# Kernel optimization log

Hardware: AMD Instinct MI355X
Metric: run time of the kernel (lower is better)

The kernel has to match this reference:

```python
import jax, jax.numpy as jnp
import numpy as np

B = 8192       # batch
HID = 1024     # hidden_dim
HEADS = 8      # head_count
OBS, ACT, N_AGENTS = 128, 32, 4
ENC_IN = N_AGENTS * OBS + ACT   # 544
DEC_IN = (N_AGENTS - 1) * ACT   # 96


def _linear(key, fan_in, fan_out):
    k1, k2 = jax.random.split(key)
    lim = 1.0 / np.sqrt(fan_in)
    W = jax.random.uniform(k1, (fan_in, fan_out), minval=-lim, maxval=lim, dtype=jnp.float32)
    b = jax.random.uniform(k2, (fan_out,), minval=-lim, maxval=lim, dtype=jnp.float32)
    return W, b


def setup_inputs() -> dict:
    key = jax.random.key(0)
    ks = jax.random.split(key, 10)
    s = jax.random.normal(ks[0], (B, N_AGENTS * OBS), dtype=jnp.float32)
    a = jax.random.normal(ks[1], (B, N_AGENTS * ACT), dtype=jnp.float32)
    W_enc_in, b_enc_in = _linear(ks[2], ENC_IN, HID)   # encoder_input_fc
    W_dec_in, b_dec_in = _linear(ks[3], DEC_IN, HID)   # decoder_input_fc
    W_eh, b_eh = _linear(ks[4], HID, HID)              # fc_encoder_input
    head_ks = jax.random.split(ks[5], HEADS)
    Wb = [_linear(k, HID, HID) for k in head_ks]       # fc_encoder_heads
    W_heads = jnp.stack([w for w, _ in Wb], axis=0)    # [H, HID, HID]
    b_heads = jnp.stack([b for _, b in Wb], axis=0)    # [H, HID]
    W_dh, b_dh = _linear(ks[6], HID, HID)              # fc_decoder_input
    W1, b1 = _linear(ks[7], HID, HID)                  # fc1
    W2, b2 = _linear(ks[8], HID, 1)                    # fc2
    return {"s": s, "a": a,
            "W_enc_in": W_enc_in, "b_enc_in": b_enc_in,
            "W_dec_in": W_dec_in, "b_dec_in": b_dec_in,
            "W_eh": W_eh, "b_eh": b_eh,
            "W_heads": W_heads, "b_heads": b_heads,
            "W_dh": W_dh, "b_dh": b_dh,
            "W1": W1, "b1": b1, "W2": W2, "b2": b2}


def reference(s, a, W_enc_in, b_enc_in, W_dec_in, b_dec_in, W_eh, b_eh,
              W_heads, b_heads, W_dh, b_dh, W1, b1, W2, b2):
    relu = jax.nn.relu
    # agent id = 0: own action is a[:, :ACT], others' actions are a[:, ACT:]
    enc_input = jnp.concatenate([s, a[:, :ACT]], axis=1) @ W_enc_in + b_enc_in   # [B, HID]
    dec_input = a[:, ACT:] @ W_dec_in + b_dec_in                                 # [B, HID]
    # Attention_ATT_2
    encoder_h = relu(enc_input @ W_eh + b_eh)                                    # [B, HID]
    encoder_heads = relu(jnp.einsum('bd,hde->hbe', encoder_h, W_heads)
                         + b_heads[:, None, :])                                  # [H, B, HID]
    decoder_H = relu(dec_input @ W_dh + b_dh)                                    # [B, HID]
    scores = jnp.einsum('hbd,bd->bh', encoder_heads, decoder_H)                  # [B, H]
    attn = jax.nn.softmax(scores, axis=1)                                        # [B, H]
    context = jnp.einsum('hbd,bh->bd', encoder_heads, attn)                      # [B, HID]
    x = relu(context @ W1 + b1)
    q = x @ W2 + b2                                                              # [B, 1]
    return q
```

## Files before the change

kernel.cpp:

```cpp
#include <hip/hip_runtime.h>
#include <hip/hip_bf16.h>
#include <hip/hip_fp16.h>

#define BATCH   8192
#define HID     1024
#define HEADS   8
#define BC      2048

typedef unsigned int  u32;
typedef unsigned short u16;
typedef __attribute__((ext_vector_type(8))) short bf16x8;
typedef __attribute__((ext_vector_type(4))) float f32x4;

__device__ __forceinline__ u32 pack_hi2(u32 u0, u32 u1) {
    return (u0 >> 16) | (u1 & 0xFFFF0000u);
}
__device__ __forceinline__ void split1(float x, u16& h, u16& l) {
    const u32 u = __float_as_uint(x);
    h = (u16)(u >> 16);
    const float r = x - __uint_as_float(u & 0xFFFF0000u);
    l = (u16)(__float_as_uint(r) >> 16);
}
__device__ __forceinline__ void splitA4(float4 v, uint2& hi, uint2& lo) {
    u32 u0 = __float_as_uint(v.x), u1 = __float_as_uint(v.y),
        u2 = __float_as_uint(v.z), u3 = __float_as_uint(v.w);
    float r0 = v.x - __uint_as_float(u0 & 0xFFFF0000u);
    float r1 = v.y - __uint_as_float(u1 & 0xFFFF0000u);
    float r2 = v.z - __uint_as_float(u2 & 0xFFFF0000u);
    float r3 = v.w - __uint_as_float(u3 & 0xFFFF0000u);
    hi.x = pack_hi2(u0, u1);
    hi.y = pack_hi2(u2, u3);
    lo.x = pack_hi2(__float_as_uint(r0), __float_as_uint(r1));
    lo.y = pack_hi2(__float_as_uint(r2), __float_as_uint(r3));
}

__device__ __forceinline__ void gld16(const u16* g, u16* l) {
    __builtin_amdgcn_global_load_lds(
        (const __attribute__((address_space(1))) u32*)g,
        (__attribute__((address_space(3))) u32*)l, 16, 0, 0);
}

struct WSplitArgs {
    const float* src[6];
    u16* hi[6];
    u16* lo[6];
};

__global__ __launch_bounds__(256) void split_weight_all(WSplitArgs args)
{
    const int z = blockIdx.z;
    int which, zz = 0;
    if (z < 3)       { which = z; }
    else if (z < 11) { which = 3; zz = z - 3; }
    else             { which = z - 7; }
    const int KT = (which == 4) ? 17 : (which == 5 ? 3 : 32);
    const int kt = blockIdx.x;
    if (kt >= KT) return;
    const int K = KT * 32;
    const long long zoff = (long long)zz * K * 1024;
    const float* W  = args.src[which] + zoff;
    u16* hi = args.hi[which] + zoff;
    u16* lo = args.lo[which] + zoff;

    const int n0  = blockIdx.y * 128;
    const int tid = threadIdx.x;
    const int k   = tid >> 3;
    const int ng  = (tid & 7) * 16;
    const float* src = W + (long long)(kt * 32 + k) * 1024 + n0 + ng;
    u16* dh = hi + ((long long)kt * 1024 + n0) * 32 + k;
    u16* dl = lo + ((long long)kt * 1024 + n0) * 32 + k;
#pragma unroll
    for (int t = 0; t < 4; t++) {
        const float4 v = *(const float4*)(src + t * 4);
        u16 h0, l0, h1, l1, h2, l2, h3, l3;
        split1(v.x, h0, l0); split1(v.y, h1, l1);
        split1(v.z, h2, l2); split1(v.w, h3, l3);
        const int nb = (ng + t * 4) * 32;
        dh[nb]      = h0; dl[nb]      = l0;
        dh[nb + 32] = h1; dl[nb + 32] = l1;
        dh[nb + 64] = h2; dl[nb + 64] = l2;
        dh[nb + 96] = h3; dl[nb + 96] = l3;
    }
}

#define HYB_GEOM \
    const int tid  = threadIdx.x; \
    const int lane = tid & 63; \
    const int wv   = tid >> 6; \
    const int wm   = wv >> 1, wn = wv & 1; \
    const int fr   = lane & 15; \
    const int fq   = lane >> 4; \
    const int m0   = blockIdx.y * 128; \
    const int n0   = blockIdx.x * 128; \
    const int lro2 = (lane >> 2) * 32 + (((lane & 3) ^ ((lane >> 3) & 3)) * 8); \
    const int br0  = wv * 16; \
    const int br1  = 64 + wv * 16; \
    const int fqx2 = (fq ^ ((fr >> 1) & 3)) * 8;

#define STAGE_HI(Ahp_, Bhp_, aoff_, boff_) \
    { \
        const u16* Ag_ = (Ahp_) + (aoff_); \
        const u16* Bg_ = (Bhp_) + (boff_); \
        gld16(Ag_ + br0 * 32 + lro2, &Ah[br0 * 32]); \
        gld16(Ag_ + br1 * 32 + lro2, &Ah[br1 * 32]); \
        gld16(Bg_ + br0 * 32 + lro2, &Bh[br0 * 32]); \
        gld16(Bg_ + br1 * 32 + lro2, &Bh[br1 * 32]); \
    }

#define LOAD_LO(Alp_, Blp_, aoff_, boff_, al_, bl_) \
    { \
        const u16* Al_ = (Alp_) + (aoff_); \
        const u16* Bl_ = (Blp_) + (boff_); \
        _Pragma("unroll") \
        for (int i = 0; i < 4; i++) { \
            al_[i] = *(const bf16x8*)(Al_ + (wm * 64 + i * 16 + fr) * 32 + fq * 8); \
            bl_[i] = *(const bf16x8*)(Bl_ + (wn * 64 + i * 16 + fr) * 32 + fq * 8); \
        } \
    }

#define MFMA_SLAB16(acc_, al_, bl_) \
    { \
        bf16x8 ah[4], bh[4]; \
        _Pragma("unroll") \
        for (int i = 0; i < 4; i++) { \
            ah[i] = *(const bf16x8*)&Ah[(wm * 64 + i * 16 + fr) * 32 + fqx2]; \
            bh[i] = *(const bf16x8*)&Bh[(wn * 64 + i * 16 + fr) * 32 + fqx2]; \
        } \
        _Pragma("unroll") \
        for (int i = 0; i < 4; i++) \
            _Pragma("unroll") \
            for (int j = 0; j < 4; j++) { \
                acc_[i][j] = __builtin_amdgcn_mfma_f32_16x16x32_bf16(ah[i], bh[j], acc_[i][j], 0, 0, 0); \
                acc_[i][j] = __builtin_amdgcn_mfma_f32_16x16x32_bf16(ah[i], bl_[j], acc_[i][j], 0, 0, 0); \
                acc_[i][j] = __builtin_amdgcn_mfma_f32_16x16x32_bf16(al_[i], bh[j], acc_[i][j], 0, 0, 0); \
            } \
    }

template <int RELU, int OUTP>
__global__ __launch_bounds__(256) void gemm_fast(
    const u16* __restrict__ Ahp, const u16* __restrict__ Alp, int MA, int moff,
    const u16* __restrict__ Bhp, const u16* __restrict__ Blp,
    const float* __restrict__ bias,
    float* __restrict__ Cf,
    u16* __restrict__ Chp, u16* __restrict__ Clp, int MC,
    int K)
{
    __shared__ alignas(16) u16 Ah[4096], Bh[4096];
    HYB_GEOM

    f32x4 acc[4][4];
#pragma unroll
    for (int i = 0; i < 4; i++)
#pragma unroll
        for (int j = 0; j < 4; j++) acc[i][j] = 0;

    const int KT = K >> 5;
    for (int kt = 0; kt < KT; kt++) {
        const long long aoff = ((long long)kt * MA + moff + m0) * 32;
        const long long boff = ((long long)kt * 1024 + n0) * 32;
        STAGE_HI(Ahp, Bhp, aoff, boff);
        bf16x8 al[4], bl[4];
        LOAD_LO(Alp, Blp, aoff, boff, al, bl);
        __syncthreads();
        MFMA_SLAB16(acc, al, bl);
        __syncthreads();
    }

#pragma unroll
    for (int j = 0; j < 4; j++) {
        const int n = n0 + wn * 64 + j * 16 + fr;
        const float bb = bias[n];
#pragma unroll
        for (int i = 0; i < 4; i++) {
#pragma unroll
            for (int r = 0; r < 4; r++) {
                const int m = m0 + wm * 64 + i * 16 + fq * 4 + r;
                float v = acc[i][j][r] + bb;
                if (RELU) v = fmaxf(v, 0.0f);
                if (OUTP) {
                    u16 h, l;
                    split1(v, h, l);
                    const long long d = ((long long)(n >> 5) * MC + moff + m) * 32 + (n & 31);
                    Chp[d] = h;
                    Clp[d] = l;
                } else {
                    Cf[(long long)m * 1024 + n] = v;
                }
            }
        }
    }
}

template <int RELU>
__global__ __launch_bounds__(256) void gemm_cvt(
    const float* __restrict__ src1, int lda1, int kofs1,
    const float* __restrict__ src2, int lda2, int ksplit,
    const u16* __restrict__ Bhp, const u16* __restrict__ Blp,
    const float* __restrict__ bias,
    u16* __restrict__ Chp, u16* __restrict__ Clp, int MC,
    int K)
{
    __shared__ alignas(16) u16 Ah[4096], Al[4096], Bh[4096], Bl[4096];
    const int tid  = threadIdx.x;
    const int lane = tid & 63;
    const int wv   = tid >> 6;
    const int wm   = wv >> 1, wn = wv & 1;
    const int fr   = lane & 15;
    const int fq   = lane >> 4;
    const int m0   = blockIdx.y * 128;
    const int n0   = blockIdx.x * 128;
    const int fqx  = (fq ^ (fr & 3)) * 8;
    const int lro  = (lane >> 2) * 32 + (((lane & 3) ^ ((lane >> 2) & 3)) * 8);
    const int br0  = wv * 16;
    const int br1  = 64 + wv * 16;
    const int ar   = tid >> 3;
    const int akq  = tid & 7;
    const int awoff = (((akq >> 1) ^ (ar & 3)) * 8) + (akq & 1) * 4;

    f32x4 acc[4][4];
#pragma unroll
    for (int i = 0; i < 4; i++)
#pragma unroll
        for (int j = 0; j < 4; j++) acc[i][j] = 0;

    const int KT = K >> 5;
    for (int kt = 0; kt < KT; kt++) {
        const int k0 = kt * 32;
        const float* srcp; int ldk, kc;
        if (k0 < ksplit) { srcp = src1; ldk = lda1; kc = k0 + kofs1; }
        else             { srcp = src2; ldk = lda2; kc = k0 - ksplit; }

        const u16* Bg  = Bhp + ((long long)kt * 1024 + n0) * 32;
        const u16* Bg2 = Blp + ((long long)kt * 1024 + n0) * 32;
        gld16(Bg  + br0 * 32 + lro, &Bh[br0 * 32]);
        gld16(Bg  + br1 * 32 + lro, &Bh[br1 * 32]);
        gld16(Bg2 + br0 * 32 + lro, &Bl[br0 * 32]);
        gld16(Bg2 + br1 * 32 + lro, &Bl[br1 * 32]);

#pragma unroll
        for (int it = 0; it < 4; it++) {
            const int row = ar + it * 32;
            const float4 v = *(const float4*)(srcp + (long long)(m0 + row) * ldk + kc + akq * 4);
            uint2 hi, lo;
            splitA4(v, hi, lo);
            *(uint2*)&Ah[row * 32 + awoff] = hi;
            *(uint2*)&Al[row * 32 + awoff] = lo;
        }
        __syncthreads();

        bf16x8 ah[4], al[4], bh[4], bl[4];
#pragma unroll
        for (int i = 0; i < 4; i++) {
            const int off = (wm * 64 + i * 16 + fr) * 32 + fqx;
            ah[i] = *(const bf16x8*)&Ah[off];
            al[i] = *(const bf16x8*)&Al[off];
        }
#pragma unroll
        for (int j = 0; j < 4; j++) {
            const int off = (wn * 64 + j * 16 + fr) * 32 + fqx;
            bh[j] = *(const bf16x8*)&Bh[off];
            bl[j] = *(const bf16x8*)&Bl[off];
        }
#pragma unroll
        for (int i = 0; i < 4; i++)
#pragma unroll
            for (int j = 0; j < 4; j++) {
                acc[i][j] = __builtin_amdgcn_mfma_f32_16x16x32_bf16(ah[i], bh[j], acc[i][j], 0, 0, 0);
                acc[i][j] = __builtin_amdgcn_mfma_f32_16x16x32_bf16(ah[i], bl[j], acc[i][j], 0, 0, 0);
                acc[i][j] = __builtin_amdgcn_mfma_f32_16x16x32_bf16(al[i], bh[j], acc[i][j], 0, 0, 0);
            }
        __syncthreads();
    }

#pragma unroll
    for (int j = 0; j < 4; j++) {
        const int n = n0 + wn * 64 + j * 16 + fr;
        const float bb = bias[n];
#pragma unroll
        for (int i = 0; i < 4; i++) {
#pragma unroll
            for (int r = 0; r < 4; r++) {
                const int m = m0 + wm * 64 + i * 16 + fq * 4 + r;
                float v = acc[i][j][r] + bb;
                if (RELU) v = fmaxf(v, 0.0f);
                u16 h, l;
                split1(v, h, l);
                const long long d = ((long long)(n >> 5) * MC + m) * 32 + (n & 31);
                Chp[d] = h;
                Clp[d] = l;
            }
        }
    }
}

__global__ __launch_bounds__(256) void heads_kernel(
    const u16* __restrict__ Ahp, const u16* __restrict__ Alp, int MA, int moff,
    const u16* __restrict__ Whp, const u16* __restrict__ Wlp,
    const float* __restrict__ b_heads,
    const float* __restrict__ decH,
    __half* __restrict__ headsb,
    float* __restrict__ scoresp)
{
    __shared__ alignas(16) u16 Ah[4096], Bh[4096];
    __shared__ float scred[2][128];
    HYB_GEOM
    const int h = blockIdx.z;
    const u16* Bhp = Whp + (long long)h * 1048576;
    const u16* Blp = Wlp + (long long)h * 1048576;
    const float* bias = b_heads + h * 1024;

    f32x4 acc[4][4];
#pragma unroll
    for (int i = 0; i < 4; i++)
#pragma unroll
        for (int j = 0; j < 4; j++) acc[i][j] = 0;

    for (int kt = 0; kt < 32; kt++) {
        const long long aoff = ((long long)kt * MA + moff + m0) * 32;
        const long long boff = ((long long)kt * 1024 + n0) * 32;
        STAGE_HI(Ahp, Bhp, aoff, boff);
        bf16x8 al[4], bl[4];
        LOAD_LO(Alp, Blp, aoff, boff, al, bl);
        __syncthreads();
        MFMA_SLAB16(acc, al, bl);
        __syncthreads();
    }

    float part[4][4];
#pragma unroll
    for (int i = 0; i < 4; i++)
#pragma unroll
        for (int r = 0; r < 4; r++) part[i][r] = 0.0f;

#pragma unroll
    for (int j = 0; j < 4; j++) {
        const int n = n0 + wn * 64 + j * 16 + fr;
        const float bb = bias[n];
#pragma unroll
        for (int i = 0; i < 4; i++) {
#pragma unroll
            for (int r = 0; r < 4; r++) {
                const int b_loc = m0 + wm * 64 + i * 16 + fq * 4 + r;
                const float v = fmaxf(acc[i][j][r] + bb, 0.0f);
                headsb[((long long)b_loc * HEADS + h) * 1024 + n] = __float2half(v);
                part[i][r] = fmaf(v, decH[(long long)b_loc * 1024 + n], part[i][r]);
            }
        }
    }
#pragma unroll
    for (int off = 1; off < 16; off <<= 1)
#pragma unroll
        for (int i = 0; i < 4; i++)
#pragma unroll
            for (int r = 0; r < 4; r++)
                part[i][r] += __shfl_xor(part[i][r], off, 64);

    if (fr == 0) {
#pragma unroll
        for (int i = 0; i < 4; i++)
#pragma unroll
            for (int r = 0; r < 4; r++)
                scred[wn][wm * 64 + i * 16 + fq * 4 + r] = part[i][r];
    }
    __syncthreads();
    if (tid < 128) {
        const float sv = scred[0][tid] + scred[1][tid];
        scoresp[(long long)(h * 8 + blockIdx.x) * BC + m0 + tid] = sv;
    }
}

__global__ __launch_bounds__(256) void context_kernel(
    const __half* __restrict__ headsb, const float* __restrict__ scoresp,
    u16* __restrict__ ctx_hi, u16* __restrict__ ctx_lo, int MC, int row0)
{
    __shared__ float sc_s[64];
    __shared__ float attn_s[HEADS];
    const int b = blockIdx.x;
    const int tid = threadIdx.x;
    if (tid < 64) sc_s[tid] = scoresp[(long long)tid * BC + b];
    __syncthreads();
    if (tid == 0) {
        float sc[HEADS];
#pragma unroll
        for (int h = 0; h < HEADS; h++) {
            float s = 0.0f;
#pragma unroll
            for (int nt = 0; nt < 8; nt++) s += sc_s[h * 8 + nt];
            sc[h] = s;
        }
        float mx = sc[0];
#pragma unroll
        for (int h = 1; h < HEADS; h++) mx = fmaxf(mx, sc[h]);
        float e[HEADS], sum = 0.0f;
#pragma unroll
        for (int h = 0; h < HEADS; h++) { e[h] = __expf(sc[h] - mx); sum += e[h]; }
        const float inv = 1.0f / sum;
#pragma unroll
        for (int h = 0; h < HEADS; h++) attn_s[h] = e[h] * inv;
    }
    __syncthreads();

    const int d = tid * 4;
    float w[HEADS];
#pragma unroll
    for (int h = 0; h < HEADS; h++) w[h] = attn_s[h];
    float4 acc = make_float4(0.f, 0.f, 0.f, 0.f);
#pragma unroll
    for (int h = 0; h < HEADS; h++) {
        const __half2* hp = (const __half2*)(headsb + ((long long)b * HEADS + h) * 1024 + d);
        const float2 f0 = __half22float2(hp[0]);
        const float2 f1 = __half22float2(hp[1]);
        acc.x = fmaf(w[h], f0.x, acc.x);
        acc.y = fmaf(w[h], f0.y, acc.y);
        acc.z = fmaf(w[h], f1.x, acc.z);
        acc.w = fmaf(w[h], f1.y, acc.w);
    }
    uint2 hi, lo;
    splitA4(acc, hi, lo);
    const long long off = ((long long)(d >> 5) * MC + row0 + b) * 32 + (d & 31);
    *(uint2*)(ctx_hi + off) = hi;
    *(uint2*)(ctx_lo + off) = lo;
}

__global__ __launch_bounds__(256) void fc2_kernel(
    const float* __restrict__ x, const float* __restrict__ W2,
    const float* __restrict__ b2, float* __restrict__ q)
{
    const int b   = blockIdx.x;
    const int tid = threadIdx.x;
    __shared__ float red[4];

    const float4 xv = *(const float4*)(x + (long long)b * 1024 + tid * 4);
    const float4 wv = *(const float4*)(W2 + tid * 4);
    float p = xv.x * wv.x + xv.y * wv.y + xv.z * wv.z + xv.w * wv.w;
#pragma unroll
    for (int off = 32; off > 0; off >>= 1) p += __shfl_down(p, off, 64);
    if ((tid & 63) == 0) red[tid >> 6] = p;
    __syncthreads();
    if (tid == 0) q[b] = red[0] + red[1] + red[2] + red[3] + b2[0];
}

extern "C" void kernel_launch(void* const* d_in, const int* in_sizes, int n_in,
                              void* d_out, int out_size, void* d_ws, size_t ws_size,
                              hipStream_t stream)
{
    const float* s        = (const float*)d_in[0];
    const float* a        = (const float*)d_in[1];
    const float* W_enc_in = (const float*)d_in[2];
    const float* b_enc_in = (const float*)d_in[3];
    const float* W_dec_in = (const float*)d_in[4];
    const float* b_dec_in = (const float*)d_in[5];
    const float* W_eh     = (const float*)d_in[6];
    const float* b_eh     = (const float*)d_in[7];
    const float* W_heads  = (const float*)d_in[8];
    const float* b_heads  = (const float*)d_in[9];
    const float* W_dh     = (const float*)d_in[10];
    const float* b_dh     = (const float*)d_in[11];
    const float* W1       = (const float*)d_in[12];
    const float* b1       = (const float*)d_in[13];
    const float* W2       = (const float*)d_in[14];
    const float* b2       = (const float*)d_in[15];
    float* q_out = (float*)d_out;

    u16* P = (u16*)d_ws;
    u16* enc_hi = P; P += 557056;
    u16* enc_lo = P; P += 557056;
    u16* dec_hi = P; P += 98304;
    u16* dec_lo = P; P += 98304;
    u16* eh_hi  = P; P += 1048576;
    u16* eh_lo  = P; P += 1048576;
    u16* dh_hi  = P; P += 1048576;
    u16* dh_lo  = P; P += 1048576;
    u16* w1_hi  = P; P += 1048576;
    u16* w1_lo  = P; P += 1048576;
    u16* wh_hi  = P; P += 8388608;
    u16* wh_lo  = P; P += 8388608;
    char* act = (char*)P;

    const dim3 blk(256);

    WSplitArgs wa;
    wa.src[0] = W_eh;    wa.hi[0] = eh_hi;  wa.lo[0] = eh_lo;
    wa.src[1] = W_dh;    wa.hi[1] = dh_hi;  wa.lo[1] = dh_lo;
    wa.src[2] = W1;      wa.hi[2] = w1_hi;  wa.lo[2] = w1_lo;
    wa.src[3] = W_heads; wa.hi[3] = wh_hi;  wa.lo[3] = wh_lo;
    wa.src[4] = W_enc_in; wa.hi[4] = enc_hi; wa.lo[4] = enc_lo;
    wa.src[5] = W_dec_in; wa.hi[5] = dec_hi; wa.lo[5] = dec_lo;
    split_weight_all<<<dim3(32, 8, 13), blk, 0, stream>>>(wa);

    const bool high = (ws_size >= 150011904ULL);

    if (high) {
        u16*    bufA_hi = (u16*)act;
        u16*    bufA_lo = bufA_hi + 8388608;
        __half* headsb  = (__half*)act;
        u16*    encH_hi = (u16*)(act + 33554432);
        u16*    encH_lo = encH_hi + 8388608;
        float*  decH    = (float*)(act + 2LL * 33554432);
        float*  scoresp = (float*)(act + 3LL * 33554432);

        const dim3 gg(8, 64, 1);
        gemm_cvt<0><<<gg, blk, 0, stream>>>(s, 512, 0, a, 128, 512,
            enc_hi, enc_lo, b_enc_in, bufA_hi, bufA_lo, 8192, 544);
        gemm_fast<1, 1><<<gg, blk, 0, stream>>>(bufA_hi, bufA_lo, 8192, 0,
            eh_hi, eh_lo, b_eh, nullptr, encH_hi, encH_lo, 8192, 1024);
        gemm_cvt<0><<<gg, blk, 0, stream>>>(a, 128, 32, a, 128, 1 << 28,
            dec_hi, dec_lo, b_dec_in, bufA_hi, bufA_lo, 8192, 96);
        gemm_fast<1, 0><<<gg, blk, 0, stream>>>(bufA_hi, bufA_lo, 8192, 0,
            dh_hi, dh_lo, b_dh, decH, nullptr, nullptr, 0, 1024);

        for (int c = 0; c < BATCH / BC; c++) {
            heads_kernel<<<dim3(8, BC / 128, 8), blk, 0, stream>>>(
                encH_hi, encH_lo, 8192, c * BC, wh_hi, wh_lo, b_heads,
                decH + (long long)c * BC * 1024, headsb, scoresp);
            context_kernel<<<dim3(BC), blk, 0, stream>>>(
                headsb, scoresp, encH_hi, encH_lo, 8192, c * BC);
        }
        gemm_fast<1, 0><<<gg, blk, 0, stream>>>(encH_hi, encH_lo, 8192, 0,
            w1_hi, w1_lo, b1, decH, nullptr, nullptr, 0, 1024);
        fc2_kernel<<<dim3(BATCH), blk, 0, stream>>>(decH, W2, b2, q_out);
    } else {
        __half* headsb  = (__half*)act;
        u16*    bufA_hi = (u16*)act;
        u16*    bufA_lo = bufA_hi + 2097152;
        u16*    encH_hi = (u16*)(act + 33554432);
        u16*    encH_lo = encH_hi + 2097152;
        float*  decH    = (float*)(act + 33554432 + 8388608);
        float*  scoresp = (float*)(act + 33554432 + 2LL * 8388608);

        const dim3 gg(8, BC / 128, 1);
        for (int c = 0; c < BATCH / BC; c++) {
            const float* sC = s + (long long)c * BC * 512;
            const float* aC = a + (long long)c * BC * 128;
            gemm_cvt<0><<<gg, blk, 0, stream>>>(sC, 512, 0, aC, 128, 512,
                enc_hi, enc_lo, b_enc_in, bufA_hi, bufA_lo, BC, 544);
            gemm_fast<1, 1><<<gg, blk, 0, stream>>>(bufA_hi, bufA_lo, BC, 0,
                eh_hi, eh_lo, b_eh, nullptr, encH_hi, encH_lo, BC, 1024);
            gemm_cvt<0><<<gg, blk, 0, stream>>>(aC, 128, 32, aC, 128, 1 << 28,
                dec_hi, dec_lo, b_dec_in, bufA_hi, bufA_lo, BC, 96);
            gemm_fast<1, 0><<<gg, blk, 0, stream>>>(bufA_hi, bufA_lo, BC, 0,
                dh_hi, dh_lo, b_dh, decH, nullptr, nullptr, 0, 1024);
            heads_kernel<<<dim3(8, BC / 128, 8), blk, 0, stream>>>(
                encH_hi, encH_lo, BC, 0, wh_hi, wh_lo, b_heads,
                decH, headsb, scoresp);
            context_kernel<<<dim3(BC), blk, 0, stream>>>(
                headsb, scoresp, encH_hi, encH_lo, BC, 0);
            gemm_fast<1, 0><<<gg, blk, 0, stream>>>(encH_hi, encH_lo, BC, 0,
                w1_hi, w1_lo, b1, decH, nullptr, nullptr, 0, 1024);
            fc2_kernel<<<dim3(BC), blk, 0, stream>>>(decH, W2, b2, q_out + (long long)c * BC);
        }
    }
}
```

Before: 779.2 us.

## Triple-buffer LDS pipeline with 256x128 tiles and 512-thread blocks for GEMMs

Replaces the single-buffered synchronous K loop in gemm_fast and heads_kernel with a three-stage LDS ring. Both hi and lo bf16 halves are loaded asynchronously two tiles ahead, and the MFMA phases are split into two half-tiles with barriers and s_setprio. Blocks grow to 512 threads covering 256 rows, which halves the grid and doubles B-tile reuse. This aims to hide global load latency and cut per-iteration sync stalls, at the cost of about 144KB of LDS per block, which limits occupancy to one block per CU and relies on precise vmcnt accounting.

```diff
diff --git a/kernel.cpp b/kernel.cpp
--- a/kernel.cpp
+++ b/kernel.cpp
@@ -83,61 +83,104 @@
     }
 }
 
-#define HYB_GEOM \
+#define PIPE_GEOM \
     const int tid  = threadIdx.x; \
     const int lane = tid & 63; \
     const int wv   = tid >> 6; \
     const int wm   = wv >> 1, wn = wv & 1; \
     const int fr   = lane & 15; \
     const int fq   = lane >> 4; \
-    const int m0   = blockIdx.y * 128; \
+    const int m0   = blockIdx.y * 256; \
     const int n0   = blockIdx.x * 128; \
     const int lro2 = (lane >> 2) * 32 + (((lane & 3) ^ ((lane >> 3) & 3)) * 8); \
-    const int br0  = wv * 16; \
-    const int br1  = 64 + wv * 16; \
-    const int fqx2 = (fq ^ ((fr >> 1) & 3)) * 8;
-
-#define STAGE_HI(Ahp_, Bhp_, aoff_, boff_) \
-    { \
-        const u16* Ag_ = (Ahp_) + (aoff_); \
-        const u16* Bg_ = (Bhp_) + (boff_); \
-        gld16(Ag_ + br0 * 32 + lro2, &Ah[br0 * 32]); \
-        gld16(Ag_ + br1 * 32 + lro2, &Ah[br1 * 32]); \
-        gld16(Bg_ + br0 * 32 + lro2, &Bh[br0 * 32]); \
-        gld16(Bg_ + br1 * 32 + lro2, &Bh[br1 * 32]); \
-    }
-
-#define LOAD_LO(Alp_, Blp_, aoff_, boff_, al_, bl_) \
-    { \
-        const u16* Al_ = (Alp_) + (aoff_); \
-        const u16* Bl_ = (Blp_) + (boff_); \
+    const int fqx2 = (fq ^ ((fr >> 1) & 3)) * 8; \
+    const int wr   = wv * 16;
+
+#define PSTAGE_HI(dst_, aoff_, boff_) { \
+    u16* db_ = (dst_); \
+    gld16(Ahp + (aoff_) + (long long)wr * 32 + lro2, db_ + wr * 32); \
+    gld16(Ahp + (aoff_) + (long long)(128 + wr) * 32 + lro2, db_ + (128 + wr) * 32); \
+    gld16(Bhp + (boff_) + (long long)wr * 32 + lro2, db_ + 16384 + wr * 32); }
+
+#define PSTAGE_LO(dst_, aoff_, boff_) { \
+    u16* db_ = (dst_); \
+    gld16(Alp + (aoff_) + (long long)wr * 32 + lro2, db_ + 8192 + wr * 32); \
+    gld16(Alp + (aoff_) + (long long)(128 + wr) * 32 + lro2, db_ + 8192 + (128 + wr) * 32); \
+    gld16(Blp + (boff_) + (long long)wr * 32 + lro2, db_ + 20480 + wr * 32); }
+
+#define PTILE(t_, STAGE0_, STAGE1_, TAILWAIT_) { \
+    const u16* bufp = smem + ((t_) % 3) * 24576; \
+    bf16x8 bh[4], bl[4], ah0[2], al0[2], ah1[2], al1[2]; \
+    _Pragma("unroll") \
+    for (int j = 0; j < 4; j++) { \
+        const int off = (wn * 64 + j * 16 + fr) * 32 + fqx2; \
+        bh[j] = *(const bf16x8*)(bufp + 16384 + off); \
+        bl[j] = *(const bf16x8*)(bufp + 20480 + off); } \
+    _Pragma("unroll") \
+    for (int i = 0; i < 2; i++) { \
+        const int off = (wm * 64 + i * 16 + fr) * 32 + fqx2; \
+        ah0[i] = *(const bf16x8*)(bufp + off); \
+        al0[i] = *(const bf16x8*)(bufp + 8192 + off); } \
+    STAGE0_; \
+    __builtin_amdgcn_s_barrier(); \
+    __builtin_amdgcn_s_setprio(1); \
+    _Pragma("unroll") \
+    for (int i = 0; i < 2; i++) \
         _Pragma("unroll") \
-        for (int i = 0; i < 4; i++) { \
-            al_[i] = *(const bf16x8*)(Al_ + (wm * 64 + i * 16 + fr) * 32 + fq * 8); \
-            bl_[i] = *(const bf16x8*)(Bl_ + (wn * 64 + i * 16 + fr) * 32 + fq * 8); \
-        } \
-    }
-
-#define MFMA_SLAB16(acc_, al_, bl_) \
-    { \
-        bf16x8 ah[4], bh[4]; \
+        for (int j = 0; j < 4; j++) { \
+            acc[i][j] = __builtin_amdgcn_mfma_f32_16x16x32_bf16(ah0[i], bh[j], acc[i][j], 0, 0, 0); \
+            acc[i][j] = __builtin_amdgcn_mfma_f32_16x16x32_bf16(ah0[i], bl[j], acc[i][j], 0, 0, 0); \
+            acc[i][j] = __builtin_amdgcn_mfma_f32_16x16x32_bf16(al0[i], bh[j], acc[i][j], 0, 0, 0); } \
+    __builtin_amdgcn_s_setprio(0); \
+    __builtin_amdgcn_s_barrier(); \
+    __builtin_amdgcn_sched_barrier(0); \
+    _Pragma("unroll") \
+    for (int i = 0; i < 2; i++) { \
+        const int off = (wm * 64 + (2 + i) * 16 + fr) * 32 + fqx2; \
+        ah1[i] = *(const bf16x8*)(bufp + off); \
+        al1[i] = *(const bf16x8*)(bufp + 8192 + off); } \
+    STAGE1_; \
+    __builtin_amdgcn_s_barrier(); \
+    __builtin_amdgcn_s_setprio(1); \
+    _Pragma("unroll") \
+    for (int i = 0; i < 2; i++) \
         _Pragma("unroll") \
-        for (int i = 0; i < 4; i++) { \
-            ah[i] = *(const bf16x8*)&Ah[(wm * 64 + i * 16 + fr) * 32 + fqx2]; \
-            bh[i] = *(const bf16x8*)&Bh[(wn * 64 + i * 16 + fr) * 32 + fqx2]; \
-        } \
-        _Pragma("unroll") \
-        for (int i = 0; i < 4; i++) \
-            _Pragma("unroll") \
-            for (int j = 0; j < 4; j++) { \
-                acc_[i][j] = __builtin_amdgcn_mfma_f32_16x16x32_bf16(ah[i], bh[j], acc_[i][j], 0, 0, 0); \
-                acc_[i][j] = __builtin_amdgcn_mfma_f32_16x16x32_bf16(ah[i], bl_[j], acc_[i][j], 0, 0, 0); \
-                acc_[i][j] = __builtin_amdgcn_mfma_f32_16x16x32_bf16(al_[i], bh[j], acc_[i][j], 0, 0, 0); \
-            } \
-    }
+        for (int j = 0; j < 4; j++) { \
+            acc[2 + i][j] = __builtin_amdgcn_mfma_f32_16x16x32_bf16(ah1[i], bh[j], acc[2 + i][j], 0, 0, 0); \
+            acc[2 + i][j] = __builtin_amdgcn_mfma_f32_16x16x32_bf16(ah1[i], bl[j], acc[2 + i][j], 0, 0, 0); \
+            acc[2 + i][j] = __builtin_amdgcn_mfma_f32_16x16x32_bf16(al1[i], bh[j], acc[2 + i][j], 0, 0, 0); } \
+    __builtin_amdgcn_s_setprio(0); \
+    TAILWAIT_; \
+    __builtin_amdgcn_s_barrier(); \
+    __builtin_amdgcn_sched_barrier(0); \
+}
+
+#define PIPE_LOOP \
+    const int KT = K >> 5; \
+    const long long astep = (long long)MA * 32; \
+    const long long bstep = 32768; \
+    const long long abase = ((long long)moff + m0) * 32; \
+    const long long bbase = (long long)n0 * 32; \
+    PSTAGE_HI(smem, abase, bbase); \
+    PSTAGE_LO(smem, abase, bbase); \
+    PSTAGE_HI(smem + 24576, abase + astep, bbase + bstep); \
+    PSTAGE_LO(smem + 24576, abase + astep, bbase + bstep); \
+    asm volatile("s_waitcnt vmcnt(6)" ::: "memory"); \
+    __builtin_amdgcn_s_barrier(); \
+    __builtin_amdgcn_sched_barrier(0); \
+    for (int t = 0; t < KT - 2; t++) { \
+        u16* dst2 = smem + ((t + 2) % 3) * 24576; \
+        const long long a2 = abase + (long long)(t + 2) * astep; \
+        const long long b2 = bbase + (long long)(t + 2) * bstep; \
+        PTILE(t, PSTAGE_HI(dst2, a2, b2), PSTAGE_LO(dst2, a2, b2), \
+              asm volatile("s_waitcnt vmcnt(6)" ::: "memory")); \
+    } \
+    PTILE(KT - 2, ((void)0), ((void)0), \
+          asm volatile("s_waitcnt vmcnt(0)" ::: "memory")); \
+    PTILE(KT - 1, ((void)0), ((void)0), ((void)0));
 
 template <int RELU, int OUTP>
-__global__ __launch_bounds__(256) void gemm_fast(
+__global__ __launch_bounds__(512) void gemm_fast(
     const u16* __restrict__ Ahp, const u16* __restrict__ Alp, int MA, int moff,
     const u16* __restrict__ Bhp, const u16* __restrict__ Blp,
     const float* __restrict__ bias,
@@ -145,8 +188,8 @@
     u16* __restrict__ Chp, u16* __restrict__ Clp, int MC,
     int K)
 {
-    __shared__ alignas(16) u16 Ah[4096], Bh[4096];
-    HYB_GEOM
+    __shared__ alignas(16) u16 smem[3 * 24576];
+    PIPE_GEOM
 
     f32x4 acc[4][4];
 #pragma unroll
@@ -154,17 +197,7 @@
 #pragma unroll
         for (int j = 0; j < 4; j++) acc[i][j] = 0;
 
-    const int KT = K >> 5;
-    for (int kt = 0; kt < KT; kt++) {
-        const long long aoff = ((long long)kt * MA + moff + m0) * 32;
-        const long long boff = ((long long)kt * 1024 + n0) * 32;
-        STAGE_HI(Ahp, Bhp, aoff, boff);
-        bf16x8 al[4], bl[4];
-        LOAD_LO(Alp, Blp, aoff, boff, al, bl);
-        __syncthreads();
-        MFMA_SLAB16(acc, al, bl);
-        __syncthreads();
-    }
+    PIPE_LOOP
 
 #pragma unroll
     for (int j = 0; j < 4; j++) {
@@ -188,6 +221,74 @@
                 }
             }
         }
+    }
+}
+
+__global__ __launch_bounds__(512) void heads_kernel(
+    const u16* __restrict__ Ahp, const u16* __restrict__ Alp, int MA, int moff,
+    const u16* __restrict__ Whp, const u16* __restrict__ Wlp,
+    const float* __restrict__ b_heads,
+    const float* __restrict__ decH,
+    __half* __restrict__ headsb,
+    float* __restrict__ scoresp)
+{
+    __shared__ alignas(16) u16 smem[3 * 24576];
+    __shared__ float scred[2][256];
+    PIPE_GEOM
+    const int h = blockIdx.z;
+    const u16* Bhp = Whp + (long long)h * 1048576;
+    const u16* Blp = Wlp + (long long)h * 1048576;
+    const float* bias = b_heads + h * 1024;
+    const int K = 1024;
+
+    f32x4 acc[4][4];
+#pragma unroll
+    for (int i = 0; i < 4; i++)
+#pragma unroll
+        for (int j = 0; j < 4; j++) acc[i][j] = 0;
+
+    PIPE_LOOP
+
+    float part[4][4];
+#pragma unroll
+    for (int i = 0; i < 4; i++)
+#pragma unroll
+        for (int r = 0; r < 4; r++) part[i][r] = 0.0f;
+
+#pragma unroll
+    for (int j = 0; j < 4; j++) {
+        const int n = n0 + wn * 64 + j * 16 + fr;
+        const float bb = bias[n];
+#pragma unroll
+        for (int i = 0; i < 4; i++) {
+#pragma unroll
+            for (int r = 0; r < 4; r++) {
+                const int b_loc = m0 + wm * 64 + i * 16 + fq * 4 + r;
+                const float v = fmaxf(acc[i][j][r] + bb, 0.0f);
+                headsb[((long long)b_loc * HEADS + h) * 1024 + n] = __float2half(v);
+                part[i][r] = fmaf(v, decH[(long long)b_loc * 1024 + n], part[i][r]);
+            }
+        }
+    }
+#pragma unroll
+    for (int off = 1; off < 16; off <<= 1)
+#pragma unroll
+        for (int i = 0; i < 4; i++)
+#pragma unroll
+            for (int r = 0; r < 4; r++)
+                part[i][r] += __shfl_xor(part[i][r], off, 64);
+
+    if (fr == 0) {
+#pragma unroll
+        for (int i = 0; i < 4; i++)
+#pragma unroll
+            for (int r = 0; r < 4; r++)
+                scred[wn][wm * 64 + i * 16 + fq * 4 + r] = part[i][r];
+    }
+    __syncthreads();
+    if (tid < 256) {
+        const float sv = scred[0][tid] + scred[1][tid];
+        scoresp[(long long)(h * 8 + blockIdx.x) * BC + m0 + tid] = sv;
     }
 }
 
@@ -290,82 +391,6 @@
                 Clp[d] = l;
             }
         }
-    }
-}
-
-__global__ __launch_bounds__(256) void heads_kernel(
-    const u16* __restrict__ Ahp, const u16* __restrict__ Alp, int MA, int moff,
-    const u16* __restrict__ Whp, const u16* __restrict__ Wlp,
-    const float* __restrict__ b_heads,
-    const float* __restrict__ decH,
-    __half* __restrict__ headsb,
-    float* __restrict__ scoresp)
-{
-    __shared__ alignas(16) u16 Ah[4096], Bh[4096];
-    __shared__ float scred[2][128];
-    HYB_GEOM
-    const int h = blockIdx.z;
-    const u16* Bhp = Whp + (long long)h * 1048576;
-    const u16* Blp = Wlp + (long long)h * 1048576;
-    const float* bias = b_heads + h * 1024;
-
-    f32x4 acc[4][4];
-#pragma unroll
-    for (int i = 0; i < 4; i++)
-#pragma unroll
-        for (int j = 0; j < 4; j++) acc[i][j] = 0;
-
-    for (int kt = 0; kt < 32; kt++) {
-        const long long aoff = ((long long)kt * MA + moff + m0) * 32;
-        const long long boff = ((long long)kt * 1024 + n0) * 32;
-        STAGE_HI(Ahp, Bhp, aoff, boff);
-        bf16x8 al[4], bl[4];
-        LOAD_LO(Alp, Blp, aoff, boff, al, bl);
-        __syncthreads();
-        MFMA_SLAB16(acc, al, bl);
-        __syncthreads();
-    }
-
-    float part[4][4];
-#pragma unroll
-    for (int i = 0; i < 4; i++)
-#pragma unroll
-        for (int r = 0; r < 4; r++) part[i][r] = 0.0f;
-
-#pragma unroll
-    for (int j = 0; j < 4; j++) {
-        const int n = n0 + wn * 64 + j * 16 + fr;
-        const float bb = bias[n];
-#pragma unroll
-        for (int i = 0; i < 4; i++) {
-#pragma unroll
-            for (int r = 0; r < 4; r++) {
-                const int b_loc = m0 + wm * 64 + i * 16 + fq * 4 + r;
-                const float v = fmaxf(acc[i][j][r] + bb, 0.0f);
-                headsb[((long long)b_loc * HEADS + h) * 1024 + n] = __float2half(v);
-                part[i][r] = fmaf(v, decH[(long long)b_loc * 1024 + n], part[i][r]);
-            }
-        }
-    }
-#pragma unroll
-    for (int off = 1; off < 16; off <<= 1)
-#pragma unroll
-        for (int i = 0; i < 4; i++)
-#pragma unroll
-            for (int r = 0; r < 4; r++)
-                part[i][r] += __shfl_xor(part[i][r], off, 64);
-
-    if (fr == 0) {
-#pragma unroll
-        for (int i = 0; i < 4; i++)
-#pragma unroll
-            for (int r = 0; r < 4; r++)
-                scred[wn][wm * 64 + i * 16 + fq * 4 + r] = part[i][r];
-    }
-    __syncthreads();
-    if (tid < 128) {
-        const float sv = scred[0][tid] + scred[1][tid];
-        scoresp[(long long)(h * 8 + blockIdx.x) * BC + m0 + tid] = sv;
     }
 }
 
@@ -478,6 +503,7 @@
     char* act = (char*)P;
 
     const dim3 blk(256);
+    const dim3 blk512(512);
 
     WSplitArgs wa;
     wa.src[0] = W_eh;    wa.hi[0] = eh_hi;  wa.lo[0] = eh_lo;
@@ -499,24 +525,25 @@
         float*  decH    = (float*)(act + 2LL * 33554432);
         float*  scoresp = (float*)(act + 3LL * 33554432);
 
-        const dim3 gg(8, 64, 1);
-        gemm_cvt<0><<<gg, blk, 0, stream>>>(s, 512, 0, a, 128, 512,
+        const dim3 ggc(8, 64, 1);
+        const dim3 ggf(8, 32, 1);
+        gemm_cvt<0><<<ggc, blk, 0, stream>>>(s, 512, 0, a, 128, 512,
             enc_hi, enc_lo, b_enc_in, bufA_hi, bufA_lo, 8192, 544);
-        gemm_fast<1, 1><<<gg, blk, 0, stream>>>(bufA_hi, bufA_lo, 8192, 0,
+        gemm_fast<1, 1><<<ggf, blk512, 0, stream>>>(bufA_hi, bufA_lo, 8192, 0,
             eh_hi, eh_lo, b_eh, nullptr, encH_hi, encH_lo, 8192, 1024);
-        gemm_cvt<0><<<gg, blk, 0, stream>>>(a, 128, 32, a, 128, 1 << 28,
+        gemm_cvt<0><<<ggc, blk, 0, stream>>>(a, 128, 32, a, 128, 1 << 28,
             dec_hi, dec_lo, b_dec_in, bufA_hi, bufA_lo, 8192, 96);
-        gemm_fast<1, 0><<<gg, blk, 0, stream>>>(bufA_hi, bufA_lo, 8192, 0,
+        gemm_fast<1, 0><<<ggf, blk512, 0, stream>>>(bufA_hi, bufA_lo, 8192, 0,
             dh_hi, dh_lo, b_dh, decH, nullptr, nullptr, 0, 1024);
 
         for (int c = 0; c < BATCH / BC; c++) {
-            heads_kernel<<<dim3(8, BC / 128, 8), blk, 0, stream>>>(
+            heads_kernel<<<dim3(8, BC / 256, 8), blk512, 0, stream>>>(
                 encH_hi, encH_lo, 8192, c * BC, wh_hi, wh_lo, b_heads,
                 decH + (long long)c * BC * 1024, headsb, scoresp);
             context_kernel<<<dim3(BC), blk, 0, stream>>>(
                 headsb, scoresp, encH_hi, encH_lo, 8192, c * BC);
         }
-        gemm_fast<1, 0><<<gg, blk, 0, stream>>>(encH_hi, encH_lo, 8192, 0,
+        gemm_fast<1, 0><<<ggf, blk512, 0, stream>>>(encH_hi, encH_lo, 8192, 0,
             w1_hi, w1_lo, b1, decH, nullptr, nullptr, 0, 1024);
         fc2_kernel<<<dim3(BATCH), blk, 0, stream>>>(decH, W2, b2, q_out);
     } else {
@@ -528,24 +555,25 @@
         float*  decH    = (float*)(act + 33554432 + 8388608);
         float*  scoresp = (float*)(act + 33554432 + 2LL * 8388608);
 
-        const dim3 gg(8, BC / 128, 1);
+        const dim3 ggc(8, BC / 128, 1);
+        const dim3 ggf(8, BC / 256, 1);
         for (int c = 0; c < BATCH / BC; c++) {
             const float* sC = s + (long long)c * BC * 512;
             const float* aC = a + (long long)c * BC * 128;
-            gemm_cvt<0><<<gg, blk, 0, stream>>>(sC, 512, 0, aC, 128, 512,
+            gemm_cvt<0><<<ggc, blk, 0, stream>>>(sC, 512, 0, aC, 128, 512,
                 enc_hi, enc_lo, b_enc_in, bufA_hi, bufA_lo, BC, 544);
-            gemm_fast<1, 1><<<gg, blk, 0, stream>>>(bufA_hi, bufA_lo, BC, 0,
+            gemm_fast<1, 1><<<ggf, blk512, 0, stream>>>(bufA_hi, bufA_lo, BC, 0,
                 eh_hi, eh_lo, b_eh, nullptr, encH_hi, encH_lo, BC, 1024);
-            gemm_cvt<0><<<gg, blk, 0, stream>>>(aC, 128, 32, aC, 128, 1 << 28,
+            gemm_cvt<0><<<ggc, blk, 0, stream>>>(aC, 128, 32, aC, 128, 1 << 28,
                 dec_hi, dec_lo, b_dec_in, bufA_hi, bufA_lo, BC, 96);
-            gemm_fast<1, 0><<<gg, blk, 0, stream>>>(bufA_hi, bufA_lo, BC, 0,
+            gemm_fast<1, 0><<<ggf, blk512, 0, stream>>>(bufA_hi, bufA_lo, BC, 0,
                 dh_hi, dh_lo, b_dh, decH, nullptr, nullptr, 0, 1024);
-            heads_kernel<<<dim3(8, BC / 128, 8), blk, 0, stream>>>(
+            heads_kernel<<<dim3(8, BC / 256, 8), blk512, 0, stream>>>(
                 encH_hi, encH_lo, BC, 0, wh_hi, wh_lo, b_heads,
                 decH, headsb, scoresp);
             context_kernel<<<dim3(BC), blk, 0, stream>>>(
                 headsb, scoresp, encH_hi, encH_lo, BC, 0);
-            gemm_fast<1, 0><<<gg, blk, 0, stream>>>(encH_hi, encH_lo, BC, 0,
+            gemm_fast<1, 0><<<ggf, blk512, 0, stream>>>(encH_hi, encH_lo, BC, 0,
                 w1_hi, w1_lo, b1, decH, nullptr, nullptr, 0, 1024);
             fc2_kernel<<<dim3(BC), blk, 0, stream>>>(decH, W2, b2, q_out + (long long)c * BC);
         }
```

New measurement: 757.5 us. 2.8% less time.
